# Kernel tuning notes

Measured on AMD Instinct MI355X. Metric: run time of the kernel, lower is better.

Reference implementation:

```python
import jax, jax.numpy as jnp
import numpy as np

B, S, D = 4, 2048, 512


def _dyt(x, alpha, w, b):
    return jnp.tanh(alpha * x) * w + b


def _fourier_fourier_attn(x, qr, qi, kr, ki, vr, vi, rtr, rti):
    xc = x.astype(jnp.complex64)
    qw, kw, vw, rtw = qr + 1j * qi, kr + 1j * ki, vr + 1j * vi, rtr + 1j * rti
    Xf = jnp.fft.fft(xc, axis=-1)  # [B,S,D] complex
    q = jnp.fft.fft(Xf * qw, axis=-2)
    k = jnp.fft.fft(Xf * kw, axis=-2)
    v = jnp.fft.fft(Xf * vw, axis=-2)
    rt = q / (k + 1e-12) * v
    rt = jnp.fft.ifft(rt, axis=-2) * rtw
    return jnp.fft.ifft(rt, axis=-1).real


def _fourier_sdpa(x, qr, qi, kr, ki, vr, vi):
    xc = x.astype(jnp.complex64)
    Xf = jnp.fft.fft(xc, axis=-1)
    proj = lambda w: jnp.fft.ifft(Xf * w, axis=-1).real
    q = proj(qr + 1j * qi)
    k = proj(kr + 1j * ki)
    v = proj(vr + 1j * vi)
    scores = jnp.einsum('bsd,btd->bst', q, k) / np.sqrt(D).astype(np.float32)
    attn = jax.nn.softmax(scores, axis=-1)
    return jnp.einsum('bst,btd->bsd', attn, v)


def _fourier_ffn(x, ar, ai, br, bi, bias):
    # Faithful to the source: the gelu branch is overwritten (dead code),
    # the returned value only uses the b-weighted FFT path.
    xc = x.astype(jnp.complex64)
    Xf = jnp.fft.fft(xc, axis=-1)
    h = jnp.fft.ifft(Xf * (ar + 1j * ai), axis=-1).real + bias
    h = jax.nn.gelu(h, approximate=False)  # discarded, as in the original
    return jnp.fft.ifft(Xf * (br + 1j * bi), axis=-1).real


def setup_inputs() -> dict:
    key = jax.random.key(0)
    ks = jax.random.split(key, 32)
    d = {'x': jax.random.normal(ks[0], (B, S, D), dtype=jnp.float32)}
    names_real = ['a_qr', 'a_kr', 'a_vr', 'a_rtr', 'b_qr', 'b_kr', 'b_vr', 'f_ar', 'f_br']
    names_imag = ['a_qi', 'a_ki', 'a_vi', 'a_rti', 'b_qi', 'b_ki', 'b_vi', 'f_ai', 'f_bi']
    i = 1
    for n in names_real:
        d[n] = 1.0 + 0.02 * jax.random.normal(ks[i], (D,), dtype=jnp.float32); i += 1
    for n in names_imag:
        d[n] = 0.02 * jax.random.normal(ks[i], (D,), dtype=jnp.float32); i += 1
    d['f_bias'] = 0.02 * jax.random.normal(ks[i], (D,), dtype=jnp.float32); i += 1
    for p in ['dyta', 'dytb', 'dytf']:
        d[p + '_alpha'] = jnp.full((1,), 0.5, dtype=jnp.float32)
        d[p + '_w'] = 1.0 + 0.02 * jax.random.normal(ks[i], (D,), dtype=jnp.float32); i += 1
        d[p + '_b'] = 0.02 * jax.random.normal(ks[i], (D,), dtype=jnp.float32); i += 1
    return d


def reference(x, a_qr, a_qi, a_kr, a_ki, a_vr, a_vi, a_rtr, a_rti,
              dyta_alpha, dyta_w, dyta_b,
              b_qr, b_qi, b_kr, b_ki, b_vr, b_vi,
              dytb_alpha, dytb_w, dytb_b,
              f_ar, f_ai, f_br, f_bi, f_bias,
              dytf_alpha, dytf_w, dytf_b):
    # attn_a block: FourierFourierAttention(DyT(x)) + x
    x = _fourier_fourier_attn(_dyt(x, dyta_alpha, dyta_w, dyta_b),
                              a_qr, a_qi, a_kr, a_ki, a_vr, a_vi, a_rtr, a_rti) + x
    # attn_b block: FourierScaledDotProductAttention(DyT(x)) + x
    x = _fourier_sdpa(_dyt(x, dytb_alpha, dytb_w, dytb_b),
                      b_qr, b_qi, b_kr, b_ki, b_vr, b_vi) + x
    # ffn block: FourierForwardNetwork(DyT(x)) + x
    x = _fourier_ffn(_dyt(x, dytf_alpha, dytf_w, dytf_b),
                     f_ar, f_ai, f_br, f_bi, f_bias) + x
    return x
```

## Files before the change

kernel.cpp:

```cpp
#include <hip/hip_runtime.h>


typedef __attribute__((ext_vector_type(8))) __bf16 bf16x8;
typedef __attribute__((ext_vector_type(4))) float floatx4;
typedef __attribute__((ext_vector_type(8))) _Float16 halfx8;
typedef __attribute__((ext_vector_type(8))) unsigned short ushortx8;

__device__ __forceinline__ unsigned short f2bf(float x) {
    unsigned u = __float_as_uint(x);
    u = (u + 0x7fffu + ((u >> 16) & 1u)) >> 16;
    return (unsigned short)u;
}

__device__ __forceinline__ float dyt_tanh(float x) {
    float e = __expf(2.0f * x);
    return 1.0f - 2.0f / (e + 1.0f);
}

__device__ __forceinline__ void async_load16(const unsigned short* g, unsigned short* l) {
    __builtin_amdgcn_global_load_lds(
        (const __attribute__((address_space(1))) unsigned int*)g,
        (__attribute__((address_space(3))) unsigned int*)l, 16, 0, 0);
}

__device__ __forceinline__ void wtw512(float (&tc)[12], float (&ts)[12], int lane) {
    const float w = -6.28318530717958647692f / 512.0f;
#pragma unroll
    for (int j = 0; j < 4; j++) __sincosf(w * (float)(j * 64 + lane), &ts[j], &tc[j]);
#pragma unroll
    for (int j = 0; j < 2; j++) __sincosf(w * (float)(2 * (j * 64 + lane)), &ts[4 + j], &tc[4 + j]);
    __sincosf(w * (float)(4 * lane), &ts[6], &tc[6]);
    __sincosf(w * (float)(8 * (lane & 31)), &ts[7], &tc[7]);
    __sincosf(w * (float)(16 * (lane & 15)), &ts[8], &tc[8]);
    __sincosf(w * (float)(32 * (lane & 7)), &ts[9], &tc[9]);
    __sincosf(w * (float)(64 * (lane & 3)), &ts[10], &tc[10]);
    __sincosf(w * (float)(128 * (lane & 1)), &ts[11], &tc[11]);
}

template <bool INV>
__device__ __forceinline__ void wfft512(float (&re)[8], float (&im)[8],
                                        const float (&tc)[12], const float (&ts)[12], int lane) {
    if (!INV) {
#pragma unroll
        for (int j = 0; j < 4; j++) {
            float ur = re[j], ui = im[j], vr = re[j + 4], vi = im[j + 4];
            re[j] = ur + vr; im[j] = ui + vi;
            float dr = ur - vr, di = ui - vi;
            re[j + 4] = dr * tc[j] - di * ts[j];
            im[j + 4] = dr * ts[j] + di * tc[j];
        }
#pragma unroll
        for (int g = 0; g < 8; g += 4)
#pragma unroll
            for (int jj = 0; jj < 2; jj++) {
                int j = g + jj;
                float ur = re[j], ui = im[j], vr = re[j + 2], vi = im[j + 2];
                re[j] = ur + vr; im[j] = ui + vi;
                float dr = ur - vr, di = ui - vi;
                re[j + 2] = dr * tc[4 + jj] - di * ts[4 + jj];
                im[j + 2] = dr * ts[4 + jj] + di * tc[4 + jj];
            }
#pragma unroll
        for (int j = 0; j < 8; j += 2) {
            float ur = re[j], ui = im[j], vr = re[j + 1], vi = im[j + 1];
            re[j] = ur + vr; im[j] = ui + vi;
            float dr = ur - vr, di = ui - vi;
            re[j + 1] = dr * tc[6] - di * ts[6];
            im[j + 1] = dr * ts[6] + di * tc[6];
        }
#pragma unroll
        for (int st = 0; st < 6; st++) {
            int h = 32 >> st;
            bool hi = (lane & h) != 0;
            float c = (st < 5) ? tc[7 + st] : 1.0f;
            float s = (st < 5) ? ts[7 + st] : 0.0f;
#pragma unroll
            for (int j = 0; j < 8; j++) {
                float orr = __shfl_xor(re[j], h, 64);
                float oii = __shfl_xor(im[j], h, 64);
                float dr = orr - re[j], di = oii - im[j];
                float sr = re[j] + orr, si = im[j] + oii;
                re[j] = hi ? (dr * c - di * s) : sr;
                im[j] = hi ? (dr * s + di * c) : si;
            }
        }
    } else {
#pragma unroll
        for (int st = 5; st >= 0; st--) {
            int h = 32 >> st;
            bool hi = (lane & h) != 0;
            float c = (st < 5) ? tc[7 + st] : 1.0f;
            float s = (st < 5) ? ts[7 + st] : 0.0f;
#pragma unroll
            for (int j = 0; j < 8; j++) {
                float zr = re[j], zi = im[j];
                float vr = zr * c + zi * s;
                float vi = zi * c - zr * s;
                float mr = hi ? vr : zr;
                float mi = hi ? vi : zi;
                float orr = __shfl_xor(mr, h, 64);
                float oii = __shfl_xor(mi, h, 64);
                re[j] = hi ? (orr - vr) : (zr + orr);
                im[j] = hi ? (oii - vi) : (zi + oii);
            }
        }
#pragma unroll
        for (int j = 0; j < 8; j += 2) {
            float vr = re[j + 1] * tc[6] + im[j + 1] * ts[6];
            float vi = im[j + 1] * tc[6] - re[j + 1] * ts[6];
            re[j + 1] = re[j] - vr; im[j + 1] = im[j] - vi;
            re[j] += vr; im[j] += vi;
        }
#pragma unroll
        for (int g = 0; g < 8; g += 4)
#pragma unroll
            for (int jj = 0; jj < 2; jj++) {
                int j = g + jj;
                float vr = re[j + 2] * tc[4 + jj] + im[j + 2] * ts[4 + jj];
                float vi = im[j + 2] * tc[4 + jj] - re[j + 2] * ts[4 + jj];
                re[j + 2] = re[j] - vr; im[j + 2] = im[j] - vi;
                re[j] += vr; im[j] += vi;
            }
#pragma unroll
        for (int j = 0; j < 4; j++) {
            float vr = re[j + 4] * tc[j] + im[j + 4] * ts[j];
            float vi = im[j + 4] * tc[j] - re[j + 4] * ts[j];
            re[j + 4] = re[j] - vr; im[j + 4] = im[j] - vi;
            re[j] += vr; im[j] += vi;
        }
    }
}

__global__ __launch_bounds__(256) void k1_dyt_fftd(
        const float* __restrict__ x,
        const float* __restrict__ alpha, const float* __restrict__ w, const float* __restrict__ bia,
        float2* __restrict__ xfC) {
    int tid = threadIdx.x, lane = tid & 63, wv = tid >> 6;
    size_t row = (size_t)blockIdx.x * 4 + wv;
    float tc[12], ts[12];
    wtw512(tc, ts, lane);
    float re[8], im[8];
    float a = alpha[0];
    const float* xr = x + row * 512;
#pragma unroll
    for (int j = 0; j < 8; j++) {
        int d = j * 64 + lane;
        re[j] = dyt_tanh(a * xr[d]) * w[d] + bia[d];
        im[j] = 0.f;
    }
    wfft512<false>(re, im, tc, ts, lane);
#pragma unroll
    for (int j = 0; j < 8; j++) {
        int d = j * 64 + lane;
        xfC[row * 512 + d] = make_float2(re[j], im[j]);
    }
}

__device__ __forceinline__ int pidx4(int i) { return i + (i >> 3); }

__device__ __forceinline__ void r4_fwd(float4* X, int t, int h) {
    int pos = t & (h - 1);
    int i = ((t & ~(h - 1)) << 2) | pos;
    int i0 = pidx4(i), i1 = pidx4(i + h), i2 = pidx4(i + 2 * h), i3 = pidx4(i + 3 * h);
    float4 a0 = X[i0], a1 = X[i1], a2 = X[i2], a3 = X[i3];
    float s1, c1;
    __sincosf(-6.28318530717958647692f * (float)pos / (float)(4 * h), &s1, &c1);
    float c2 = c1 * c1 - s1 * s1, s2 = 2.f * c1 * s1;
    float c3 = c2 * c1 - s2 * s1, s3 = s2 * c1 + c2 * s1;
    float4 o0, o1, o2, o3;
    {
        float t0r = a0.x + a2.x, t0i = a0.y + a2.y, t1r = a0.x - a2.x, t1i = a0.y - a2.y;
        float t2r = a1.x + a3.x, t2i = a1.y + a3.y, t3r = a1.x - a3.x, t3i = a1.y - a3.y;
        o0.x = t0r + t2r; o0.y = t0i + t2i;
        float b1r = t1r + t3i, b1i = t1i - t3r;
        float b2r = t0r - t2r, b2i = t0i - t2i;
        float b3r = t1r - t3i, b3i = t1i + t3r;
        o1.x = b1r * c1 - b1i * s1; o1.y = b1r * s1 + b1i * c1;
        o2.x = b2r * c2 - b2i * s2; o2.y = b2r * s2 + b2i * c2;
        o3.x = b3r * c3 - b3i * s3; o3.y = b3r * s3 + b3i * c3;
    }
    {
        float t0r = a0.z + a2.z, t0i = a0.w + a2.w, t1r = a0.z - a2.z, t1i = a0.w - a2.w;
        float t2r = a1.z + a3.z, t2i = a1.w + a3.w, t3r = a1.z - a3.z, t3i = a1.w - a3.w;
        o0.z = t0r + t2r; o0.w = t0i + t2i;
        float b1r = t1r + t3i, b1i = t1i - t3r;
        float b2r = t0r - t2r, b2i = t0i - t2i;
        float b3r = t1r - t3i, b3i = t1i + t3r;
        o1.z = b1r * c1 - b1i * s1; o1.w = b1r * s1 + b1i * c1;
        o2.z = b2r * c2 - b2i * s2; o2.w = b2r * s2 + b2i * c2;
        o3.z = b3r * c3 - b3i * s3; o3.w = b3r * s3 + b3i * c3;
    }
    X[i0] = o0; X[i1] = o1; X[i2] = o2; X[i3] = o3;
}

__device__ __forceinline__ void r4_inv(float4* X, int t, int h) {
    int pos = t & (h - 1);
    int i = ((t & ~(h - 1)) << 2) | pos;
    int i0 = pidx4(i), i1 = pidx4(i + h), i2 = pidx4(i + 2 * h), i3 = pidx4(i + 3 * h);
    float4 y0 = X[i0], y1 = X[i1], y2 = X[i2], y3 = X[i3];
    float s1, c1;
    __sincosf(-6.28318530717958647692f * (float)pos / (float)(4 * h), &s1, &c1);
    float c2 = c1 * c1 - s1 * s1, s2 = 2.f * c1 * s1;
    float c3 = c2 * c1 - s2 * s1, s3 = s2 * c1 + c2 * s1;
    float4 o0, o1, o2, o3;
    {
        float u1r = y1.x * c1 + y1.y * s1, u1i = y1.y * c1 - y1.x * s1;
        float u2r = y2.x * c2 + y2.y * s2, u2i = y2.y * c2 - y2.x * s2;
        float u3r = y3.x * c3 + y3.y * s3, u3i = y3.y * c3 - y3.x * s3;
        float s0r = y0.x + u2r, s0i = y0.y + u2i;
        float s1r = y0.x - u2r, s1i = y0.y - u2i;
        float s2r = u1r + u3r, s2i = u1i + u3i;
        float s3r = u1r - u3r, s3i = u1i - u3i;
        o0.x = s0r + s2r; o0.y = s0i + s2i;
        o2.x = s0r - s2r; o2.y = s0i - s2i;
        o1.x = s1r - s3i; o1.y = s1i + s3r;
        o3.x = s1r + s3i; o3.y = s1i - s3r;
    }
    {
        float u1r = y1.z * c1 + y1.w * s1, u1i = y1.w * c1 - y1.z * s1;
        float u2r = y2.z * c2 + y2.w * s2, u2i = y2.w * c2 - y2.z * s2;
        float u3r = y3.z * c3 + y3.w * s3, u3i = y3.w * c3 - y3.z * s3;
        float s0r = y0.z + u2r, s0i = y0.w + u2i;
        float s1r = y0.z - u2r, s1i = y0.w - u2i;
        float s2r = u1r + u3r, s2i = u1i + u3i;
        float s3r = u1r - u3r, s3i = u1i - u3i;
        o0.z = s0r + s2r; o0.w = s0i + s2i;
        o2.z = s0r - s2r; o2.w = s0i - s2i;
        o1.z = s1r - s3i; o1.w = s1i + s3r;
        o3.z = s1r + s3i; o3.w = s1i - s3r;
    }
    X[i0] = o0; X[i1] = o1; X[i2] = o2; X[i3] = o3;
}

__global__ __launch_bounds__(512) void k2_sfft(
        float2* __restrict__ xfC,
        const float* __restrict__ qr, const float* __restrict__ qi,
        const float* __restrict__ kr, const float* __restrict__ ki,
        const float* __restrict__ vr, const float* __restrict__ vi,
        const float* __restrict__ rtr, const float* __restrict__ rti) {
    __shared__ float4 buf[2304];
    int t = threadIdx.x;
    int g = blockIdx.x;
    int xcd = g & 7, r = g >> 3;
    int pp = xcd * 32 + (r & 31);
    int b = r >> 5;
    int p0 = pp * 2;
    float4* colg = (float4*)(xfC + (size_t)b * 2048 * 512 + p0);

#pragma unroll
    for (int c = 0; c < 4; c++) {
        int s = t + 512 * c;
        buf[pidx4(s)] = colg[(size_t)s * 256];
    }
    __syncthreads(); r4_fwd(buf, t, 512);
    __syncthreads(); r4_fwd(buf, t, 128);
    __syncthreads(); r4_fwd(buf, t, 32);
    __syncthreads(); r4_fwd(buf, t, 8);
    __syncthreads(); r4_fwd(buf, t, 2);
    __syncthreads();
#pragma unroll
    for (int c = 0; c < 2; c++) {
        int pr = t + 512 * c;
        int ia = pidx4(2 * pr), ib = pidx4(2 * pr + 1);
        float4 a = buf[ia], bb = buf[ib];
        buf[ia] = make_float4(a.x + bb.x, a.y + bb.y, a.z + bb.z, a.w + bb.w);
        buf[ib] = make_float4(a.x - bb.x, a.y - bb.y, a.z - bb.z, a.w - bb.w);
    }
    __syncthreads();

    int f0 = __brev((unsigned)p0) >> 23;
    int f1 = __brev((unsigned)(p0 + 1)) >> 23;
    float qw0r = qr[f0], qw0i = qi[f0], kw0r = kr[f0], kw0i = ki[f0], vw0r = vr[f0], vw0i = vi[f0];
    float qw1r = qr[f1], qw1i = qi[f1], kw1r = kr[f1], kw1i = ki[f1], vw1r = vr[f1], vw1i = vi[f1];
#pragma unroll
    for (int c = 0; c < 4; c++) {
        int idx = pidx4(t + 512 * c);
        float4 y = buf[idx];
        {
            float yr = y.x, yi = y.y;
            float qre = yr * qw0r - yi * qw0i, qim = yr * qw0i + yi * qw0r;
            float kre = yr * kw0r - yi * kw0i + 1e-12f, kim = yr * kw0i + yi * kw0r;
            float vre = yr * vw0r - yi * vw0i, vim = yr * vw0i + yi * vw0r;
            float inv = 1.0f / (kre * kre + kim * kim);
            float dre = (qre * kre + qim * kim) * inv;
            float dim = (qim * kre - qre * kim) * inv;
            y.x = dre * vre - dim * vim;
            y.y = dre * vim + dim * vre;
        }
        {
            float yr = y.z, yi = y.w;
            float qre = yr * qw1r - yi * qw1i, qim = yr * qw1i + yi * qw1r;
            float kre = yr * kw1r - yi * kw1i + 1e-12f, kim = yr * kw1i + yi * kw1r;
            float vre = yr * vw1r - yi * vw1i, vim = yr * vw1i + yi * vw1r;
            float inv = 1.0f / (kre * kre + kim * kim);
            float dre = (qre * kre + qim * kim) * inv;
            float dim = (qim * kre - qre * kim) * inv;
            y.z = dre * vre - dim * vim;
            y.w = dre * vim + dim * vre;
        }
        buf[idx] = y;
    }

    __syncthreads();
#pragma unroll
    for (int c = 0; c < 2; c++) {
        int pr = t + 512 * c;
        int ia = pidx4(2 * pr), ib = pidx4(2 * pr + 1);
        float4 a = buf[ia], bb = buf[ib];
        buf[ia] = make_float4(a.x + bb.x, a.y + bb.y, a.z + bb.z, a.w + bb.w);
        buf[ib] = make_float4(a.x - bb.x, a.y - bb.y, a.z - bb.z, a.w - bb.w);
    }
    __syncthreads(); r4_inv(buf, t, 2);
    __syncthreads(); r4_inv(buf, t, 8);
    __syncthreads(); r4_inv(buf, t, 32);
    __syncthreads(); r4_inv(buf, t, 128);
    __syncthreads(); r4_inv(buf, t, 512);
    __syncthreads();

    const float sc = 1.0f / 2048.0f;
    float r0r = rtr[f0] * sc, r0i = rti[f0] * sc;
    float r1r = rtr[f1] * sc, r1i = rti[f1] * sc;
#pragma unroll
    for (int c = 0; c < 4; c++) {
        int s = t + 512 * c;
        float4 z = buf[pidx4(s)];
        float4 o;
        o.x = z.x * r0r - z.y * r0i; o.y = z.x * r0i + z.y * r0r;
        o.z = z.z * r1r - z.w * r1i; o.w = z.z * r1i + z.w * r1r;
        colg[(size_t)s * 256] = o;
    }
}

__global__ __launch_bounds__(256) void k3_mid(
        const float2* __restrict__ xfC,
        const float* __restrict__ x,
        const float* __restrict__ alpha, const float* __restrict__ w, const float* __restrict__ bia,
        const float* __restrict__ qr, const float* __restrict__ qi,
        const float* __restrict__ kr, const float* __restrict__ ki,
        const float* __restrict__ vr, const float* __restrict__ vi,
        float* __restrict__ x1,
        unsigned short* __restrict__ qb, unsigned short* __restrict__ kb, unsigned short* __restrict__ vb) {
    __shared__ __align__(16) char smem[4 * 1024 * 8];
    int tid = threadIdx.x, lane = tid & 63, wv = tid >> 6;
    float2* zb = (float2*)(smem + wv * 8192);
    float* wbs = (float*)smem;
    float2* zf = (float2*)(smem + 12288 + wv * 4096);
    size_t pr = (size_t)blockIdx.x * 4 + wv;
    size_t r1 = pr * 2, r2 = r1 + 1;
    float tc[12], ts[12];
    wtw512(tc, ts, lane);

    float xa[8], xb2[8];
#pragma unroll
    for (int j = 0; j < 8; j++) {
        int d = j * 64 + lane;
        zb[d]       = xfC[r1 * 512 + d];
        zb[512 + d] = xfC[r2 * 512 + d];
        xa[j]  = x[r1 * 512 + d];
        xb2[j] = x[r2 * 512 + d];
    }
    float re[8], im[8];
#pragma unroll
    for (int j = 0; j < 8; j++) {
        int d = j * 64 + lane;
        int fd = __brev((unsigned)d) >> 23;
        int dp = __brev((unsigned)((512 - fd) & 511)) >> 23;
        float2 z1 = zb[d], z1p = zb[dp];
        float2 z2 = zb[512 + d], z2p = zb[512 + dp];
        float h1r = 0.5f * (z1.x + z1p.x), h1i = 0.5f * (z1.y - z1p.y);
        float h2r = 0.5f * (z2.x + z2p.x), h2i = 0.5f * (z2.y - z2p.y);
        re[j] = h1r - h2i;
        im[j] = h1i + h2r;
    }
    __syncthreads();
    for (int idx = tid; idx < 512; idx += 256) {
        int f = __brev((unsigned)idx) >> 23;
        int gg = (512 - f) & 511;
        float aa = (f == 0 || f == 256) ? 0.04419417382415922f : 0.0625f;
        float ah = aa * 0.5f;
        const float s5 = 0.5f * (1.0f / 512.0f);
        wbs[0 * 512 + idx] = ah * (qr[f] + qr[gg]); wbs[1 * 512 + idx] = ah * (qi[f] - qi[gg]);
        wbs[2 * 512 + idx] = ah * (kr[f] + kr[gg]); wbs[3 * 512 + idx] = ah * (ki[f] - ki[gg]);
        wbs[4 * 512 + idx] = s5 * (vr[f] + vr[gg]); wbs[5 * 512 + idx] = s5 * (vi[f] - vi[gg]);
    }

    wfft512<true>(re, im, tc, ts, lane);
    float a = alpha[0];
    float gre[8], gim[8];
#pragma unroll
    for (int j = 0; j < 8; j++) {
        int d = j * 64 + lane;
        float v1 = re[j] * (1.0f / 512.0f) + xa[j];
        float v2 = im[j] * (1.0f / 512.0f) + xb2[j];
        x1[r1 * 512 + d] = v1;
        x1[r2 * 512 + d] = v2;
        gre[j] = dyt_tanh(a * v1) * w[d] + bia[d];
        gim[j] = dyt_tanh(a * v2) * w[d] + bia[d];
    }
    wfft512<false>(gre, gim, tc, ts, lane);
    __syncthreads();

#pragma unroll
    for (int j = 0; j < 8; j++)
        zf[j * 64 + lane] = make_float2(gre[j], gim[j]);

    float pvr[8], pvi[8];
#pragma unroll
    for (int j = 0; j < 8; j++) {
        int i = j * 64 + lane;
        float wr0 = wbs[4 * 512 + i], wi0 = wbs[5 * 512 + i];
        pvr[j] = gre[j] * wr0 - gim[j] * wi0;
        pvi[j] = gre[j] * wi0 + gim[j] * wr0;
    }

    bool odd = (lane & 1) != 0;
#pragma unroll
    for (int j = 0; j < 8; j++) {
        int d = j * 64 + lane;
        int fd = __brev((unsigned)d) >> 23;
        int dp = __brev((unsigned)((512 - fd) & 511)) >> 23;
        float2 Zp = zf[dp];
        float zr = gre[j], zi = gim[j];
        float A1r = 0.5f * (zr + Zp.x), A1i = 0.5f * (zi - Zp.y);
        float A2r = 0.5f * (zi + Zp.y), A2i = 0.5f * (Zp.x - zr);
        float wr0 = wbs[0 * 512 + d], wi0 = wbs[1 * 512 + d];
        float Q1r = A1r * wr0 - A1i * wi0, Q1i = A1r * wi0 + A1i * wr0;
        float Q2r = A2r * wr0 - A2i * wi0, Q2i = A2r * wi0 + A2i * wr0;
        qb[r1 * 512 + d] = f2bf(odd ? -Q1i : Q1r);
        qb[r2 * 512 + d] = f2bf(odd ? -Q2i : Q2r);
        float wr1 = wbs[2 * 512 + d], wi1 = wbs[3 * 512 + d];
        float K1r = A1r * wr1 - A1i * wi1, K1i = A1r * wi1 + A1i * wr1;
        float K2r = A2r * wr1 - A2i * wi1, K2i = A2r * wi1 + A2i * wr1;
        kb[r1 * 512 + d] = f2bf(odd ? -K1i : K1r);
        kb[r2 * 512 + d] = f2bf(odd ? -K2i : K2r);
    }

    wfft512<true>(pvr, pvi, tc, ts, lane);
#pragma unroll
    for (int j = 0; j < 8; j++) {
        int d = j * 64 + lane;
        vb[r1 * 512 + d] = f2bf(pvr[j]);
        vb[r2 * 512 + d] = f2bf(pvi[j]);
    }
}

__global__ __launch_bounds__(256) void ktr_transpose(
        const unsigned short* __restrict__ vb, unsigned short* __restrict__ vT) {
    __shared__ unsigned short tile[64][65];
    int b = blockIdx.z;
    int s0 = blockIdx.x * 64;
    int d0 = blockIdx.y * 64;
    int tx = threadIdx.x & 63, ty = threadIdx.x >> 6;
    for (int j = 0; j < 16; j++) {
        int s = ty + j * 4;
        tile[s][tx] = vb[((size_t)b * 2048 + s0 + s) * 512 + d0 + tx];
    }
    __syncthreads();
    for (int j = 0; j < 16; j++) {
        int d = ty + j * 4;
        vT[((size_t)b * 512 + d0 + d) * 2048 + s0 + tx] = tile[tx][d];
    }
}

__global__ __launch_bounds__(256) void gemm_bt(
        const unsigned short* __restrict__ A, const unsigned short* __restrict__ Bt,
        void* __restrict__ C, int M, int N, int Ks, int kseg, float scale, int out_half) {
    int tilesM = M >> 7, tilesN = N >> 7;
    int perBatch = tilesM * tilesN;
    int l = blockIdx.x;
    int seg = blockIdx.y;
    int s = l & 7, t = l >> 3;
    int cnt = perBatch >> 3;
    int bz = t / cnt;
    int u = t - bz * cnt;
    int pn = tilesN >> 1, pm = tilesM >> 2;
    int n0 = ((s & 1) * pn + (u % pn)) << 7;
    int m0 = ((s >> 1) * pm + (u / pn)) << 7;
    int kbase = seg * kseg;

    const unsigned short* Ab = A + (size_t)bz * M * Ks;
    const unsigned short* Bb = Bt + (size_t)bz * N * Ks;
    __shared__ __align__(16) unsigned short smem[2 * 128 * 64];
    unsigned short* As = smem;
    unsigned short* Bs = smem + 128 * 64;
    int tid = threadIdx.x;
    int wave = tid >> 6, lane = tid & 63;
    int wm = (wave >> 1) * 64, wn = (wave & 1) * 64;
    int lrow = lane & 15, lq = lane >> 4;
    floatx4 acc[4][4];
#pragma unroll
    for (int i = 0; i < 4; i++)
#pragma unroll
        for (int j = 0; j < 4; j++)
            acc[i][j] = (floatx4){0.f, 0.f, 0.f, 0.f};

    int lr = lane >> 3;
    int lcs = lane & 7;
    for (int k0 = kbase; k0 < kbase + kseg; k0 += 64) {
        __syncthreads();
#pragma unroll
        for (int i = 0; i < 4; i++) {
            int c = wave * 4 + i;
            int r = c * 8 + lr;
            int gcol = ((lcs ^ (r & 7)) << 3);
            async_load16(Ab + (size_t)(m0 + r) * Ks + k0 + gcol, As + c * 512);
            async_load16(Bb + (size_t)(n0 + r) * Ks + k0 + gcol, Bs + c * 512);
        }
        __syncthreads();
        bf16x8 a0[4], a1[4], b0[4], b1[4];
#pragma unroll
        for (int mi = 0; mi < 4; mi++) {
            int r = wm + mi * 16 + lrow;
            a0[mi] = *(const bf16x8*)(As + r * 64 + ((lq ^ (r & 7)) << 3));
            a1[mi] = *(const bf16x8*)(As + r * 64 + (((lq + 4) ^ (r & 7)) << 3));
        }
#pragma unroll
        for (int ni = 0; ni < 4; ni++) {
            int r = wn + ni * 16 + lrow;
            b0[ni] = *(const bf16x8*)(Bs + r * 64 + ((lq ^ (r & 7)) << 3));
            b1[ni] = *(const bf16x8*)(Bs + r * 64 + (((lq + 4) ^ (r & 7)) << 3));
        }
#pragma unroll
        for (int mi = 0; mi < 4; mi++)
#pragma unroll
            for (int ni = 0; ni < 4; ni++) {
                acc[mi][ni] = __builtin_amdgcn_mfma_f32_16x16x32_bf16(a0[mi], b0[ni], acc[mi][ni], 0, 0, 0);
                acc[mi][ni] = __builtin_amdgcn_mfma_f32_16x16x32_bf16(a1[mi], b1[ni], acc[mi][ni], 0, 0, 0);
            }
    }
    size_t cbase = ((size_t)seg * 4 + bz) * (size_t)M * N;
    int lr0 = (wave >> 1) * 16 + lq * 4;
    for (int mi = 0; mi < 4; mi++) {
        __syncthreads();
        if (out_half) {
            _Float16* Cs = (_Float16*)smem;
            for (int ni = 0; ni < 4; ni++)
                for (int r = 0; r < 4; r++)
                    Cs[(lr0 + r) * 128 + wn + ni * 16 + lrow] = (_Float16)(acc[mi][ni][r] * scale);
            __syncthreads();
            for (int h = 0; h < 2; h++) {
                int chunk = tid + h * 256;
                int rl = chunk >> 4, cb = (chunk & 15) * 16;
                int grow = m0 + mi * 16 + (rl & 15) + (rl >> 4) * 64;
                *(uint4*)((char*)C + (cbase + (size_t)grow * N + n0) * 2 + cb) =
                    *(const uint4*)((const char*)Cs + rl * 256 + cb);
            }
        } else {
            float* Cs = (float*)smem;
            for (int ni = 0; ni < 4; ni++)
                for (int r = 0; r < 4; r++)
                    Cs[(lr0 + r) * 128 + wn + ni * 16 + lrow] = acc[mi][ni][r] * scale;
            __syncthreads();
            for (int h = 0; h < 4; h++) {
                int chunk = tid + h * 256;
                int rl = chunk >> 5, cb = (chunk & 31) * 16;
                int grow = m0 + mi * 16 + (rl & 15) + (rl >> 4) * 64;
                *(uint4*)((char*)C + (cbase + (size_t)grow * N + n0) * 4 + cb) =
                    *(const uint4*)((const char*)Cs + rl * 512 + cb);
            }
        }
    }
}

__global__ __launch_bounds__(256) void softmax_rows(
        const _Float16* __restrict__ Sc, unsigned short* __restrict__ P) {
    __shared__ float red[4];
    int tid = threadIdx.x;
    size_t row = blockIdx.x;
    halfx8 hv = *(const halfx8*)(Sc + row * 2048 + tid * 8);
    float v[8];
#pragma unroll
    for (int j = 0; j < 8; j++) v[j] = (float)hv[j];
    float mx = v[0];
#pragma unroll
    for (int j = 1; j < 8; j++) mx = fmaxf(mx, v[j]);
    for (int off = 32; off >= 1; off >>= 1) mx = fmaxf(mx, __shfl_xor(mx, off));
    int wv = tid >> 6;
    if ((tid & 63) == 0) red[wv] = mx;
    __syncthreads();
    mx = fmaxf(fmaxf(red[0], red[1]), fmaxf(red[2], red[3]));
    float e[8], sum = 0.f;
#pragma unroll
    for (int j = 0; j < 8; j++) { e[j] = __expf(v[j] - mx); sum += e[j]; }
    for (int off = 32; off >= 1; off >>= 1) sum += __shfl_xor(sum, off);
    __syncthreads();
    if ((tid & 63) == 0) red[wv] = sum;
    __syncthreads();
    float inv = 1.0f / (red[0] + red[1] + red[2] + red[3]);
    ushortx8 o;
#pragma unroll
    for (int j = 0; j < 8; j++) o[j] = f2bf(e[j] * inv);
    *(ushortx8*)(P + row * 2048 + tid * 8) = o;
}

__global__ __launch_bounds__(256) void k5_ffn(
        const float* __restrict__ attn0, const float* __restrict__ attn1,
        const float* __restrict__ x1,
        const float* __restrict__ alpha, const float* __restrict__ w, const float* __restrict__ bia,
        const float* __restrict__ br, const float* __restrict__ bi,
        float* __restrict__ out) {
    __shared__ float wbs[2][512];
    int tid = threadIdx.x, lane = tid & 63, wv = tid >> 6;
    size_t pr = (size_t)blockIdx.x * 4 + wv;
    size_t r1 = pr * 2, r2 = r1 + 1;
    for (int idx = tid; idx < 512; idx += 256) {
        int f = __brev((unsigned)idx) >> 23;
        int gg = (512 - f) & 511;
        wbs[0][idx] = 0.5f * (br[f] + br[gg]) * (1.0f / 512.0f);
        wbs[1][idx] = 0.5f * (bi[f] - bi[gg]) * (1.0f / 512.0f);
    }
    float tc[12], ts[12];
    wtw512(tc, ts, lane);
    float a = alpha[0];
    float re[8], im[8], x2a[8], x2b[8];
#pragma unroll
    for (int j = 0; j < 8; j++) {
        int d = j * 64 + lane;
        float v1 = attn0[r1 * 512 + d] + attn1[r1 * 512 + d] + x1[r1 * 512 + d];
        float v2 = attn0[r2 * 512 + d] + attn1[r2 * 512 + d] + x1[r2 * 512 + d];
        x2a[j] = v1; x2b[j] = v2;
        re[j] = dyt_tanh(a * v1) * w[d] + bia[d];
        im[j] = dyt_tanh(a * v2) * w[d] + bia[d];
    }
    wfft512<false>(re, im, tc, ts, lane);
    __syncthreads();
#pragma unroll
    for (int j = 0; j < 8; j++) {
        int i = j * 64 + lane;
        float wr0 = wbs[0][i], wi0 = wbs[1][i];
        float rr = re[j], ii = im[j];
        re[j] = rr * wr0 - ii * wi0;
        im[j] = rr * wi0 + ii * wr0;
    }
    wfft512<true>(re, im, tc, ts, lane);
#pragma unroll
    for (int j = 0; j < 8; j++) {
        int d = j * 64 + lane;
        out[r1 * 512 + d] = re[j] + x2a[j];
        out[r2 * 512 + d] = im[j] + x2b[j];
    }
}

extern "C" void kernel_launch(void* const* d_in, const int* in_sizes, int n_in,
                              void* d_out, int out_size, void* d_ws, size_t ws_size,
                              hipStream_t stream) {
    const float* x      = (const float*)d_in[0];
    const float* a_qr   = (const float*)d_in[1];
    const float* a_kr   = (const float*)d_in[2];
    const float* a_vr   = (const float*)d_in[3];
    const float* a_rtr  = (const float*)d_in[4];
    const float* b_qr   = (const float*)d_in[5];
    const float* b_kr   = (const float*)d_in[6];
    const float* b_vr   = (const float*)d_in[7];
    const float* f_br   = (const float*)d_in[9];
    const float* a_qi   = (const float*)d_in[10];
    const float* a_ki   = (const float*)d_in[11];
    const float* a_vi   = (const float*)d_in[12];
    const float* a_rti  = (const float*)d_in[13];
    const float* b_qi   = (const float*)d_in[14];
    const float* b_ki   = (const float*)d_in[15];
    const float* b_vi   = (const float*)d_in[16];
    const float* f_bi   = (const float*)d_in[18];
    const float* dyta_alpha = (const float*)d_in[20];
    const float* dyta_w     = (const float*)d_in[21];
    const float* dyta_b     = (const float*)d_in[22];
    const float* dytb_alpha = (const float*)d_in[23];
    const float* dytb_w     = (const float*)d_in[24];
    const float* dytb_b     = (const float*)d_in[25];
    const float* dytf_alpha = (const float*)d_in[26];
    const float* dytf_w     = (const float*)d_in[27];
    const float* dytf_b     = (const float*)d_in[28];
    (void)in_sizes; (void)n_in; (void)out_size; (void)ws_size;

    char* ws = (char*)d_ws;
    const size_t MB = 1024 * 1024;
    float2* xfC = (float2*)(ws + 0 * MB);
    float* x1   = (float*)(ws + 32 * MB);
    unsigned short* qb = (unsigned short*)(ws + 48 * MB);
    unsigned short* kb = (unsigned short*)(ws + 56 * MB);
    unsigned short* vb = (unsigned short*)(ws + 64 * MB);
    unsigned short* vT = (unsigned short*)(ws + 72 * MB);
    _Float16* scores   = (_Float16*)(ws + 0 * MB);
    unsigned short* Pb = (unsigned short*)(ws + 0 * MB);
    float* attnP       = (float*)(ws + 81 * MB);
    float* outp = (float*)d_out;

    k1_dyt_fftd<<<2048, 256, 0, stream>>>(x, dyta_alpha, dyta_w, dyta_b, xfC);
    k2_sfft<<<1024, 512, 0, stream>>>(xfC, a_qr, a_qi, a_kr, a_ki, a_vr, a_vi, a_rtr, a_rti);
    k3_mid<<<1024, 256, 0, stream>>>(xfC, x, dytb_alpha, dytb_w, dytb_b,
                                     b_qr, b_qi, b_kr, b_ki, b_vr, b_vi, x1, qb, kb, vb);
    ktr_transpose<<<dim3(32, 8, 4), 256, 0, stream>>>(vb, vT);
    gemm_bt<<<1024, 256, 0, stream>>>(qb, kb, scores, 2048, 2048, 512, 512,
                                      0.04419417382415922f, 1);
    softmax_rows<<<8192, 256, 0, stream>>>(scores, Pb);
    gemm_bt<<<dim3(256, 2), 256, 0, stream>>>(Pb, vT, attnP, 2048, 512, 2048, 1024,
                                              1.0f, 0);
    k5_ffn<<<1024, 256, 0, stream>>>(attnP, attnP + (size_t)4 * 2048 * 512, x1,
                                     dytf_alpha, dytf_w, dytf_b, f_br, f_bi, outp);
}
```

Measured before the change: 295.1 us.

## Store FFT intermediates in fp16, tabulate twiddles in LDS, merge transpose into softmax

```diff
diff --git a/kernel.cpp b/kernel.cpp
--- a/kernel.cpp
+++ b/kernel.cpp
@@ -5,6 +5,8 @@
 typedef __attribute__((ext_vector_type(4))) float floatx4;
 typedef __attribute__((ext_vector_type(8))) _Float16 halfx8;
 typedef __attribute__((ext_vector_type(8))) unsigned short ushortx8;
+typedef __attribute__((ext_vector_type(2))) _Float16 half2v;
+typedef __attribute__((ext_vector_type(4))) _Float16 half4v;
 
 __device__ __forceinline__ unsigned short f2bf(float x) {
     unsigned u = __float_as_uint(x);
@@ -134,7 +136,7 @@
 __global__ __launch_bounds__(256) void k1_dyt_fftd(
         const float* __restrict__ x,
         const float* __restrict__ alpha, const float* __restrict__ w, const float* __restrict__ bia,
-        float2* __restrict__ xfC) {
+        half2v* __restrict__ xf) {
     int tid = threadIdx.x, lane = tid & 63, wv = tid >> 6;
     size_t row = (size_t)blockIdx.x * 4 + wv;
     float tc[12], ts[12];
@@ -152,19 +154,19 @@
 #pragma unroll
     for (int j = 0; j < 8; j++) {
         int d = j * 64 + lane;
-        xfC[row * 512 + d] = make_float2(re[j], im[j]);
+        xf[row * 512 + d] = (half2v){(_Float16)re[j], (_Float16)im[j]};
     }
 }
 
 __device__ __forceinline__ int pidx4(int i) { return i + (i >> 3); }
 
-__device__ __forceinline__ void r4_fwd(float4* X, int t, int h) {
+__device__ __forceinline__ void r4_fwd(float4* X, int t, int h, const half2v* tw) {
     int pos = t & (h - 1);
     int i = ((t & ~(h - 1)) << 2) | pos;
     int i0 = pidx4(i), i1 = pidx4(i + h), i2 = pidx4(i + 2 * h), i3 = pidx4(i + 3 * h);
     float4 a0 = X[i0], a1 = X[i1], a2 = X[i2], a3 = X[i3];
-    float s1, c1;
-    __sincosf(-6.28318530717958647692f * (float)pos / (float)(4 * h), &s1, &c1);
+    half2v wv = tw[pos];
+    float c1 = (float)wv.x, s1 = (float)wv.y;
     float c2 = c1 * c1 - s1 * s1, s2 = 2.f * c1 * s1;
     float c3 = c2 * c1 - s2 * s1, s3 = s2 * c1 + c2 * s1;
     float4 o0, o1, o2, o3;
@@ -193,13 +195,13 @@
     X[i0] = o0; X[i1] = o1; X[i2] = o2; X[i3] = o3;
 }
 
-__device__ __forceinline__ void r4_inv(float4* X, int t, int h) {
+__device__ __forceinline__ void r4_inv(float4* X, int t, int h, const half2v* tw) {
     int pos = t & (h - 1);
     int i = ((t & ~(h - 1)) << 2) | pos;
     int i0 = pidx4(i), i1 = pidx4(i + h), i2 = pidx4(i + 2 * h), i3 = pidx4(i + 3 * h);
     float4 y0 = X[i0], y1 = X[i1], y2 = X[i2], y3 = X[i3];
-    float s1, c1;
-    __sincosf(-6.28318530717958647692f * (float)pos / (float)(4 * h), &s1, &c1);
+    half2v wv = tw[pos];
+    float c1 = (float)wv.x, s1 = (float)wv.y;
     float c2 = c1 * c1 - s1 * s1, s2 = 2.f * c1 * s1;
     float c3 = c2 * c1 - s2 * s1, s3 = s2 * c1 + c2 * s1;
     float4 o0, o1, o2, o3;
@@ -233,30 +235,46 @@
 }
 
 __global__ __launch_bounds__(512) void k2_sfft(
-        float2* __restrict__ xfC,
+        half2v* __restrict__ xf,
         const float* __restrict__ qr, const float* __restrict__ qi,
         const float* __restrict__ kr, const float* __restrict__ ki,
         const float* __restrict__ vr, const float* __restrict__ vi,
         const float* __restrict__ rtr, const float* __restrict__ rti) {
     __shared__ float4 buf[2304];
+    __shared__ half2v twd[682];
     int t = threadIdx.x;
     int g = blockIdx.x;
     int xcd = g & 7, r = g >> 3;
     int pp = xcd * 32 + (r & 31);
-    int b = r >> 5;
+    int b = r >> 3 >> 2;
+    b = r >> 5;
     int p0 = pp * 2;
-    float4* colg = (float4*)(xfC + (size_t)b * 2048 * 512 + p0);
+    half4v* colh = (half4v*)(xf + (size_t)b * 2048 * 512 + p0);
+
+    for (int i = t; i < 682; i += 512) {
+        int h, off;
+        if (i < 512)      { h = 512; off = 0; }
+        else if (i < 640) { h = 128; off = 512; }
+        else if (i < 672) { h = 32;  off = 640; }
+        else if (i < 680) { h = 8;   off = 672; }
+        else              { h = 2;   off = 680; }
+        int pos = i - off;
+        float s, c;
+        __sincosf(-6.28318530717958647692f * (float)pos / (float)(4 * h), &s, &c);
+        twd[i] = (half2v){(_Float16)c, (_Float16)s};
+    }
 
 #pragma unroll
     for (int c = 0; c < 4; c++) {
         int s = t + 512 * c;
-        buf[pidx4(s)] = colg[(size_t)s * 256];
-    }
-    __syncthreads(); r4_fwd(buf, t, 512);
-    __syncthreads(); r4_fwd(buf, t, 128);
-    __syncthreads(); r4_fwd(buf, t, 32);
-    __syncthreads(); r4_fwd(buf, t, 8);
-    __syncthreads(); r4_fwd(buf, t, 2);
+        half4v h = colh[(size_t)s * 256];
+        buf[pidx4(s)] = make_float4((float)h.x, (float)h.y, (float)h.z, (float)h.w);
+    }
+    __syncthreads(); r4_fwd(buf, t, 512, twd);
+    __syncthreads(); r4_fwd(buf, t, 128, twd + 512);
+    __syncthreads(); r4_fwd(buf, t, 32, twd + 640);
+    __syncthreads(); r4_fwd(buf, t, 8, twd + 672);
+    __syncthreads(); r4_fwd(buf, t, 2, twd + 680);
     __syncthreads();
 #pragma unroll
     for (int c = 0; c < 2; c++) {
@@ -310,11 +328,11 @@
         buf[ia] = make_float4(a.x + bb.x, a.y + bb.y, a.z + bb.z, a.w + bb.w);
         buf[ib] = make_float4(a.x - bb.x, a.y - bb.y, a.z - bb.z, a.w - bb.w);
     }
-    __syncthreads(); r4_inv(buf, t, 2);
-    __syncthreads(); r4_inv(buf, t, 8);
-    __syncthreads(); r4_inv(buf, t, 32);
-    __syncthreads(); r4_inv(buf, t, 128);
-    __syncthreads(); r4_inv(buf, t, 512);
+    __syncthreads(); r4_inv(buf, t, 2, twd + 680);
+    __syncthreads(); r4_inv(buf, t, 8, twd + 672);
+    __syncthreads(); r4_inv(buf, t, 32, twd + 640);
+    __syncthreads(); r4_inv(buf, t, 128, twd + 512);
+    __syncthreads(); r4_inv(buf, t, 512, twd);
     __syncthreads();
 
     const float sc = 1.0f / 2048.0f;
@@ -324,15 +342,14 @@
     for (int c = 0; c < 4; c++) {
         int s = t + 512 * c;
         float4 z = buf[pidx4(s)];
-        float4 o;
-        o.x = z.x * r0r - z.y * r0i; o.y = z.x * r0i + z.y * r0r;
-        o.z = z.z * r1r - z.w * r1i; o.w = z.z * r1i + z.w * r1r;
-        colg[(size_t)s * 256] = o;
+        float ox = z.x * r0r - z.y * r0i, oy = z.x * r0i + z.y * r0r;
+        float oz = z.z * r1r - z.w * r1i, ow = z.z * r1i + z.w * r1r;
+        colh[(size_t)s * 256] = (half4v){(_Float16)ox, (_Float16)oy, (_Float16)oz, (_Float16)ow};
     }
 }
 
 __global__ __launch_bounds__(256) void k3_mid(
-        const float2* __restrict__ xfC,
+        const half2v* __restrict__ xf,
         const float* __restrict__ x,
         const float* __restrict__ alpha, const float* __restrict__ w, const float* __restrict__ bia,
         const float* __restrict__ qr, const float* __restrict__ qi,
@@ -354,8 +371,10 @@
 #pragma unroll
     for (int j = 0; j < 8; j++) {
         int d = j * 64 + lane;
-        zb[d]       = xfC[r1 * 512 + d];
-        zb[512 + d] = xfC[r2 * 512 + d];
+        half2v h1 = xf[r1 * 512 + d];
+        half2v h2 = xf[r2 * 512 + d];
+        zb[d]       = make_float2((float)h1.x, (float)h1.y);
+        zb[512 + d] = make_float2((float)h2.x, (float)h2.y);
         xa[j]  = x[r1 * 512 + d];
         xb2[j] = x[r2 * 512 + d];
     }
@@ -441,24 +460,6 @@
         int d = j * 64 + lane;
         vb[r1 * 512 + d] = f2bf(pvr[j]);
         vb[r2 * 512 + d] = f2bf(pvi[j]);
-    }
-}
-
-__global__ __launch_bounds__(256) void ktr_transpose(
-        const unsigned short* __restrict__ vb, unsigned short* __restrict__ vT) {
-    __shared__ unsigned short tile[64][65];
-    int b = blockIdx.z;
-    int s0 = blockIdx.x * 64;
-    int d0 = blockIdx.y * 64;
-    int tx = threadIdx.x & 63, ty = threadIdx.x >> 6;
-    for (int j = 0; j < 16; j++) {
-        int s = ty + j * 4;
-        tile[s][tx] = vb[((size_t)b * 2048 + s0 + s) * 512 + d0 + tx];
-    }
-    __syncthreads();
-    for (int j = 0; j < 16; j++) {
-        int d = ty + j * 4;
-        vT[((size_t)b * 512 + d0 + d) * 2048 + s0 + tx] = tile[tx][d];
     }
 }
 
@@ -562,35 +563,54 @@
     }
 }
 
-__global__ __launch_bounds__(256) void softmax_rows(
-        const _Float16* __restrict__ Sc, unsigned short* __restrict__ P) {
-    __shared__ float red[4];
-    int tid = threadIdx.x;
-    size_t row = blockIdx.x;
-    halfx8 hv = *(const halfx8*)(Sc + row * 2048 + tid * 8);
-    float v[8];
-#pragma unroll
-    for (int j = 0; j < 8; j++) v[j] = (float)hv[j];
-    float mx = v[0];
-#pragma unroll
-    for (int j = 1; j < 8; j++) mx = fmaxf(mx, v[j]);
-    for (int off = 32; off >= 1; off >>= 1) mx = fmaxf(mx, __shfl_xor(mx, off));
-    int wv = tid >> 6;
-    if ((tid & 63) == 0) red[wv] = mx;
-    __syncthreads();
-    mx = fmaxf(fmaxf(red[0], red[1]), fmaxf(red[2], red[3]));
-    float e[8], sum = 0.f;
-#pragma unroll
-    for (int j = 0; j < 8; j++) { e[j] = __expf(v[j] - mx); sum += e[j]; }
-    for (int off = 32; off >= 1; off >>= 1) sum += __shfl_xor(sum, off);
-    __syncthreads();
-    if ((tid & 63) == 0) red[wv] = sum;
-    __syncthreads();
-    float inv = 1.0f / (red[0] + red[1] + red[2] + red[3]);
-    ushortx8 o;
-#pragma unroll
-    for (int j = 0; j < 8; j++) o[j] = f2bf(e[j] * inv);
-    *(ushortx8*)(P + row * 2048 + tid * 8) = o;
+__global__ __launch_bounds__(256) void sm_tr(
+        const _Float16* __restrict__ Sc, unsigned short* __restrict__ P,
+        const unsigned short* __restrict__ vb, unsigned short* __restrict__ vT) {
+    __shared__ __align__(16) char lds[64 * 65 * 2];
+    if (blockIdx.x < 8192) {
+        float* red = (float*)lds;
+        int tid = threadIdx.x;
+        size_t row = blockIdx.x;
+        halfx8 hv = *(const halfx8*)(Sc + row * 2048 + tid * 8);
+        float v[8];
+#pragma unroll
+        for (int j = 0; j < 8; j++) v[j] = (float)hv[j];
+        float mx = v[0];
+#pragma unroll
+        for (int j = 1; j < 8; j++) mx = fmaxf(mx, v[j]);
+        for (int off = 32; off >= 1; off >>= 1) mx = fmaxf(mx, __shfl_xor(mx, off));
+        int wv = tid >> 6;
+        if ((tid & 63) == 0) red[wv] = mx;
+        __syncthreads();
+        mx = fmaxf(fmaxf(red[0], red[1]), fmaxf(red[2], red[3]));
+        float e[8], sum = 0.f;
+#pragma unroll
+        for (int j = 0; j < 8; j++) { e[j] = __expf(v[j] - mx); sum += e[j]; }
+        for (int off = 32; off >= 1; off >>= 1) sum += __shfl_xor(sum, off);
+        __syncthreads();
+        if ((tid & 63) == 0) red[wv] = sum;
+        __syncthreads();
+        float inv = 1.0f / (red[0] + red[1] + red[2] + red[3]);
+        ushortx8 o;
+#pragma unroll
+        for (int j = 0; j < 8; j++) o[j] = f2bf(e[j] * inv);
+        *(ushortx8*)(P + row * 2048 + tid * 8) = o;
+    } else {
+        unsigned short (*tile)[65] = (unsigned short (*)[65])lds;
+        int id = blockIdx.x - 8192;
+        int sx = id & 31, dy = (id >> 5) & 7, bz = id >> 8;
+        int s0 = sx * 64, d0 = dy * 64;
+        int tx = threadIdx.x & 63, ty = threadIdx.x >> 6;
+        for (int j = 0; j < 16; j++) {
+            int s = ty + j * 4;
+            tile[s][tx] = vb[((size_t)bz * 2048 + s0 + s) * 512 + d0 + tx];
+        }
+        __syncthreads();
+        for (int j = 0; j < 16; j++) {
+            int d = ty + j * 4;
+            vT[((size_t)bz * 512 + d0 + d) * 2048 + s0 + tx] = tile[tx][d];
+        }
+    }
 }
 
 __global__ __launch_bounds__(256) void k5_ffn(
@@ -674,7 +694,7 @@
 
     char* ws = (char*)d_ws;
     const size_t MB = 1024 * 1024;
-    float2* xfC = (float2*)(ws + 0 * MB);
+    half2v* xfH = (half2v*)(ws + 0 * MB);
     float* x1   = (float*)(ws + 32 * MB);
     unsigned short* qb = (unsigned short*)(ws + 48 * MB);
     unsigned short* kb = (unsigned short*)(ws + 56 * MB);
@@ -685,14 +705,13 @@
     float* attnP       = (float*)(ws + 81 * MB);
     float* outp = (float*)d_out;
 
-    k1_dyt_fftd<<<2048, 256, 0, stream>>>(x, dyta_alpha, dyta_w, dyta_b, xfC);
-    k2_sfft<<<1024, 512, 0, stream>>>(xfC, a_qr, a_qi, a_kr, a_ki, a_vr, a_vi, a_rtr, a_rti);
-    k3_mid<<<1024, 256, 0, stream>>>(xfC, x, dytb_alpha, dytb_w, dytb_b,
+    k1_dyt_fftd<<<2048, 256, 0, stream>>>(x, dyta_alpha, dyta_w, dyta_b, xfH);
+    k2_sfft<<<1024, 512, 0, stream>>>(xfH, a_qr, a_qi, a_kr, a_ki, a_vr, a_vi, a_rtr, a_rti);
+    k3_mid<<<1024, 256, 0, stream>>>(xfH, x, dytb_alpha, dytb_w, dytb_b,
                                      b_qr, b_qi, b_kr, b_ki, b_vr, b_vi, x1, qb, kb, vb);
-    ktr_transpose<<<dim3(32, 8, 4), 256, 0, stream>>>(vb, vT);
     gemm_bt<<<1024, 256, 0, stream>>>(qb, kb, scores, 2048, 2048, 512, 512,
                                       0.04419417382415922f, 1);
-    softmax_rows<<<8192, 256, 0, stream>>>(scores, Pb);
+    sm_tr<<<9216, 256, 0, stream>>>(scores, Pb, vb, vT);
     gemm_bt<<<dim3(256, 2), 256, 0, stream>>>(Pb, vT, attnP, 2048, 512, 2048, 1024,
                                               1.0f, 0);
     k5_ffn<<<1024, 256, 0, stream>>>(attnP, attnP + (size_t)4 * 2048 * 512, x1,
```

Measured after the change: 284.2 us. 3.7% less time.
